# Kernel optimization log

Measured on AMD Instinct MI355X. Metric: run time of the kernel, lower is better.

The kernel has to match this reference:

```python
import jax, jax.numpy as jnp
from jax import lax
import numpy as np

B, L, C, H, W = 2, 5, 32, 48, 176
NUM_ITER = 1  # args['num_iteration']


def _affine_grid(M, Ho, Wo):
    # torch F.affine_grid, align_corners=False. M: (..., 2, 3) -> (..., Ho, Wo, 2)
    xs = (2.0 * jnp.arange(Wo, dtype=M.dtype) + 1.0) / Wo - 1.0
    ys = (2.0 * jnp.arange(Ho, dtype=M.dtype) + 1.0) / Ho - 1.0
    X, Y = jnp.meshgrid(xs, ys)  # (Ho, Wo)
    base = jnp.stack([X, Y, jnp.ones_like(X)], axis=-1)  # (Ho, Wo, 3)
    return jnp.einsum('...ij,hwj->...hwi', M, base)


def _grid_sample(img, grid):
    # torch F.grid_sample bilinear, zero padding, align_corners=False.
    # img: (C, H, W), grid: (Ho, Wo, 2) normalized coords -> (C, Ho, Wo)
    Ci, Hi, Wi = img.shape
    ix = ((grid[..., 0] + 1.0) * Wi - 1.0) * 0.5
    iy = ((grid[..., 1] + 1.0) * Hi - 1.0) * 0.5
    x0 = jnp.floor(ix)
    y0 = jnp.floor(iy)
    wx = ix - x0
    wy = iy - y0

    def tap(xf, yf):
        valid = ((xf >= 0) & (xf <= Wi - 1) & (yf >= 0) & (yf <= Hi - 1)).astype(img.dtype)
        xi = jnp.clip(xf, 0, Wi - 1).astype(jnp.int32)
        yi = jnp.clip(yf, 0, Hi - 1).astype(jnp.int32)
        return img[:, yi, xi] * valid  # (C, Ho, Wo)

    return (tap(x0, y0) * (1 - wx) * (1 - wy)
            + tap(x0 + 1, y0) * wx * (1 - wy)
            + tap(x0, y0 + 1) * (1 - wx) * wy
            + tap(x0 + 1, y0 + 1) * wx * wy)


_warp_batch = jax.vmap(_grid_sample)


def setup_inputs() -> dict:
    key = jax.random.key(0)
    ks = jax.random.split(key, 6)
    x = jax.random.normal(ks[0], (B * L, C, H, W), dtype=jnp.float32)
    record_len = jnp.full((B,), L, dtype=jnp.int64)
    eye = jnp.array([[1.0, 0.0, 0.0], [0.0, 1.0, 0.0]], dtype=jnp.float32)
    M = eye + 0.1 * jax.random.normal(ks[1], (B, L, L, 2, 3), dtype=jnp.float32)
    msg_w = jax.random.normal(ks[2], (C, 2 * C, 3, 3), dtype=jnp.float32) * (1.0 / np.sqrt(2 * C * 9))
    msg_b = jnp.zeros((C,), dtype=jnp.float32)
    mlp_w = jax.random.normal(ks[3], (C, C), dtype=jnp.float32) * (1.0 / np.sqrt(C))
    mlp_b = jnp.zeros((C,), dtype=jnp.float32)
    return {"x": x, "record_len": record_len, "normalized_affine_matrix": M,
            "msg_w": msg_w, "msg_b": msg_b, "mlp_w": mlp_w, "mlp_b": mlp_b}


def reference(x, record_len, normalized_affine_matrix, msg_w, msg_b, mlp_w, mlp_b):
    M = normalized_affine_matrix
    feat = x.reshape(B, L, C, H, W)  # regroup (record_len == L per batch)

    grids = _affine_grid(M, H, W).reshape(B * L * L, H, W, 2)

    # roi mask: warp an all-ones image with each pairwise transform
    ones_img = jnp.ones((1, H, W), dtype=x.dtype)
    mask = jax.vmap(lambda g: _grid_sample(ones_img, g))(grids)
    mask = mask.reshape(B, L, L, 1, H, W)

    for _ in range(NUM_ITER):
        # warped[b,i,j] = warp(feat[b,j], M[b,i,j])
        imgs = jnp.broadcast_to(feat[:, None], (B, L, L, C, H, W)).reshape(B * L * L, C, H, W)
        warped = _warp_batch(imgs, grids).reshape(B, L, L, C, H, W)
        ego = jnp.broadcast_to(feat[:, :, None], (B, L, L, C, H, W))
        cat = jnp.concatenate([warped, ego], axis=3).reshape(B * L * L, 2 * C, H, W)
        msg = lax.conv_general_dilated(cat, msg_w, (1, 1), ((1, 1), (1, 1)),
                                       dimension_numbers=('NCHW', 'OIHW', 'NCHW'))
        msg = msg + msg_b[None, :, None, None]
        msg = msg.reshape(B, L, L, C, H, W) * mask
        agg = jnp.max(msg, axis=2)  # 'max' agg over neighbors j -> (B, L, C, H, W)
        feat = feat + agg  # gru_flag=False branch

    out = feat[:, 0]  # ego agent feature, (B, C, H, W)
    out = jnp.einsum('bchw,dc->bdhw', out, mlp_w) + mlp_b[None, :, None, None]
    return out
```

## Files before the change

### kernel.cpp

```cpp
#include <hip/hip_runtime.h>
#include <hip/hip_bf16.h>
#include <math.h>

#define BB 2
#define LL 5
#define CC 32
#define HH 48
#define WW 176
#define HWs (HH * WW)
#define BL (BB * LL)

typedef __attribute__((ext_vector_type(8))) short bf16x8;
typedef __attribute__((ext_vector_type(4))) float f32x4;

__device__ __forceinline__ unsigned short f2bf(float v) {
    __hip_bfloat16 h = __float2bfloat16(v);
    return *reinterpret_cast<unsigned short*>(&h);
}
__device__ __forceinline__ float bf2f(unsigned short u) {
    __hip_bfloat16 h = *reinterpret_cast<__hip_bfloat16*>(&u);
    return __bfloat162float(h);
}

__device__ __forceinline__ void bilin_weights(const float* __restrict__ Mp, int h, int w,
                                              int& o00, int& o10, int& o01, int& o11,
                                              float& a00, float& a10, float& a01, float& a11)
{
    float xs = (2.0f * (float)w + 1.0f) / (float)WW - 1.0f;
    float ys = (2.0f * (float)h + 1.0f) / (float)HH - 1.0f;
    float gx = Mp[0] * xs + Mp[1] * ys + Mp[2];
    float gy = Mp[3] * xs + Mp[4] * ys + Mp[5];
    float ix = ((gx + 1.0f) * (float)WW - 1.0f) * 0.5f;
    float iy = ((gy + 1.0f) * (float)HH - 1.0f) * 0.5f;
    float x0f = floorf(ix), y0f = floorf(iy);
    float wx = ix - x0f, wy = iy - y0f;
    float x1f = x0f + 1.0f, y1f = y0f + 1.0f;
    bool vx0 = (x0f >= 0.0f) && (x0f <= (float)(WW - 1));
    bool vx1 = (x1f >= 0.0f) && (x1f <= (float)(WW - 1));
    bool vy0 = (y0f >= 0.0f) && (y0f <= (float)(HH - 1));
    bool vy1 = (y1f >= 0.0f) && (y1f <= (float)(HH - 1));
    int xi0 = (int)fminf(fmaxf(x0f, 0.0f), (float)(WW - 1));
    int xi1 = (int)fminf(fmaxf(x1f, 0.0f), (float)(WW - 1));
    int yi0 = (int)fminf(fmaxf(y0f, 0.0f), (float)(HH - 1));
    int yi1 = (int)fminf(fmaxf(y1f, 0.0f), (float)(HH - 1));
    o00 = yi0 * WW + xi0;
    o10 = yi0 * WW + xi1;
    o01 = yi1 * WW + xi0;
    o11 = yi1 * WW + xi1;
    a00 = (vx0 && vy0) ? (1.0f - wx) * (1.0f - wy) : 0.0f;
    a10 = (vx1 && vy0) ? wx * (1.0f - wy) : 0.0f;
    a01 = (vx0 && vy1) ? (1.0f - wx) * wy : 0.0f;
    a11 = (vx1 && vy1) ? wx * wy : 0.0f;
}

__global__ __launch_bounds__(256) void k_prep(const float* __restrict__ x,
                                              const float* __restrict__ M,
                                              const float* __restrict__ msg_w,
                                              const float* __restrict__ mlp_w,
                                              unsigned short* __restrict__ warpedcl,
                                              unsigned short* __restrict__ egocl,
                                              float* __restrict__ maskb,
                                              unsigned short* __restrict__ Wp,
                                              unsigned short* __restrict__ Wp2)
{
    int y = blockIdx.y;
    if (y < BL) {
        int pix = blockIdx.x * 256 + threadIdx.x;
        int cg  = blockIdx.z;
        int w = pix % WW, h = pix / WW;
        int b = y / LL, j = y % LL;
        const float* Mp = M + (size_t)(b * LL * LL + j) * 6;
        int o00, o10, o01, o11;
        float a00, a10, a01, a11;
        bilin_weights(Mp, h, w, o00, o10, o01, o11, a00, a10, a01, a11);
        if (cg == 0)
            maskb[(size_t)y * HWs + pix] = a00 + a10 + a01 + a11;
        const float* img = x + (size_t)y * CC * HWs + (size_t)cg * 8 * HWs;
        bf16x8 v8;
#pragma unroll
        for (int c = 0; c < 8; ++c) {
            const float* ip = img + (size_t)c * HWs;
            float v = a00 * ip[o00] + a10 * ip[o10] + a01 * ip[o01] + a11 * ip[o11];
            v8[c] = (short)f2bf(v);
        }
        *(bf16x8*)(warpedcl + ((size_t)y * HWs + pix) * CC + cg * 8) = v8;
    } else if (y < BL + BB) {
        int b = y - BL;
        int pix = blockIdx.x * 256 + threadIdx.x;
        int cg  = blockIdx.z;
        const float* img = x + (size_t)(b * LL) * CC * HWs + (size_t)cg * 8 * HWs;
        bf16x8 v8;
#pragma unroll
        for (int c = 0; c < 8; ++c)
            v8[c] = (short)f2bf(img[(size_t)c * HWs + pix]);
        *(bf16x8*)(egocl + ((size_t)b * HWs + pix) * CC + cg * 8) = v8;
    } else {
        int i = (blockIdx.z * gridDim.x + blockIdx.x) * 256 + threadIdx.x;
        if (i < 2 * 9 * 32 * 32) {
            int half = i / (9 * 32 * 32);
            int r    = i % (9 * 32 * 32);
            int tap  = r / (32 * 32);
            int r2   = r % (32 * 32);
            int oc   = r2 / 32;
            int ic   = r2 % 32;
            Wp[i] = f2bf(msg_w[(size_t)oc * 576 + (size_t)(half * 32 + ic) * 9 + tap]);
        } else if (i < 2 * 9 * 32 * 32 + 32 * 32) {
            int k = i - 2 * 9 * 32 * 32;
            Wp2[k] = f2bf(mlp_w[k]);
        }
    }
}

__global__ __launch_bounds__(256) void k_fused(const unsigned short* __restrict__ warpedcl,
                                               const unsigned short* __restrict__ egocl,
                                               const float* __restrict__ maskb,
                                               const unsigned short* __restrict__ Wp,
                                               const unsigned short* __restrict__ Wp2,
                                               const float* __restrict__ msg_b,
                                               const float* __restrict__ mlp_b,
                                               float* __restrict__ out)
{
    __shared__ float fl[64][33];
    int wv   = threadIdx.x >> 6;
    int lane = threadIdx.x & 63;
    int lo   = lane & 15;
    int kblk = lane >> 4;
    int b    = blockIdx.y;
    int p0   = blockIdx.x * 64 + wv * 16;
    int pf   = p0 + lo;
    int ph   = pf / WW, pw = pf % WW;

    int ps[9];
    unsigned vbits = 0;
#pragma unroll
    for (int tap = 0; tap < 9; ++tap) {
        int dy = tap / 3 - 1, dx = tap % 3 - 1;
        int hh = ph + dy, wwp = pw + dx;
        bool valid = (hh >= 0) && (hh < HH) && (wwp >= 0) && (wwp < WW);
        ps[tap] = valid ? (pf + dy * WW + dx) : pf;
        vbits |= (valid ? 1u : 0u) << tap;
    }
    const bf16x8 zero = {0, 0, 0, 0, 0, 0, 0, 0};

    bf16x8 Bw[9][2];
#pragma unroll
    for (int tap = 0; tap < 9; ++tap)
#pragma unroll
        for (int nt = 0; nt < 2; ++nt)
            Bw[tap][nt] = *(const bf16x8*)(Wp + ((size_t)(tap * 32 + nt * 16 + lo) * 32 + kblk * 8));

    f32x4 acce[2] = {};
    {
        const unsigned short* Ae = egocl + (size_t)b * HWs * CC;
#pragma unroll
        for (int tap = 0; tap < 9; ++tap) {
            bf16x8 Af = *(const bf16x8*)(Ae + (size_t)ps[tap] * CC + kblk * 8);
            if (!((vbits >> tap) & 1)) Af = zero;
#pragma unroll
            for (int nt = 0; nt < 2; ++nt) {
                bf16x8 Bf = *(const bf16x8*)(Wp + 9 * 32 * 32 + ((size_t)(tap * 32 + nt * 16 + lo) * 32 + kblk * 8));
                acce[nt] = __builtin_amdgcn_mfma_f32_16x16x32_bf16(Af, Bf, acce[nt], 0, 0, 0);
            }
        }
        float b0 = msg_b[lo], b1 = msg_b[16 + lo];
#pragma unroll
        for (int r = 0; r < 4; ++r) { acce[0][r] += b0; acce[1][r] += b1; }
    }

    f32x4 agg[2];
#pragma unroll
    for (int r = 0; r < 4; ++r) { agg[0][r] = -INFINITY; agg[1][r] = -INFINITY; }

    for (int j = 0; j < LL; ++j) {
        const unsigned short* Aw = warpedcl + (size_t)(b * LL + j) * HWs * CC;
        f32x4 acc[2] = {};
#pragma unroll
        for (int tap = 0; tap < 9; ++tap) {
            bf16x8 Af = *(const bf16x8*)(Aw + (size_t)ps[tap] * CC + kblk * 8);
            if (!((vbits >> tap) & 1)) Af = zero;
#pragma unroll
            for (int nt = 0; nt < 2; ++nt)
                acc[nt] = __builtin_amdgcn_mfma_f32_16x16x32_bf16(Af, Bw[tap][nt], acc[nt], 0, 0, 0);
        }
        float4 mk = *(const float4*)(maskb + (size_t)(b * LL + j) * HWs + p0 + kblk * 4);
        float mkr[4] = {mk.x, mk.y, mk.z, mk.w};
#pragma unroll
        for (int nt = 0; nt < 2; ++nt)
#pragma unroll
            for (int r = 0; r < 4; ++r)
                agg[nt][r] = fmaxf(agg[nt][r], (acc[nt][r] + acce[nt][r]) * mkr[r]);
    }

#pragma unroll
    for (int nt = 0; nt < 2; ++nt)
#pragma unroll
        for (int r = 0; r < 4; ++r) {
            int pixl = kblk * 4 + r;
            float skip = bf2f(egocl[((size_t)b * HWs + p0 + pixl) * CC + nt * 16 + lo]);
            float f = agg[nt][r] + skip;
            fl[wv * 16 + pixl][nt * 16 + lo] = f;
        }

    bf16x8 Afm;
#pragma unroll
    for (int e = 0; e < 8; ++e)
        Afm[e] = (short)f2bf(fl[wv * 16 + lo][kblk * 8 + e]);

#pragma unroll
    for (int nt2 = 0; nt2 < 2; ++nt2) {
        bf16x8 Bm = *(const bf16x8*)(Wp2 + ((size_t)(nt2 * 16 + lo) * 32 + kblk * 8));
        f32x4 om = {};
        om = __builtin_amdgcn_mfma_f32_16x16x32_bf16(Afm, Bm, om, 0, 0, 0);
        float mb2 = mlp_b[nt2 * 16 + lo];
        int d = nt2 * 16 + lo;
#pragma unroll
        for (int r = 0; r < 4; ++r)
            out[((size_t)b * CC + d) * HWs + p0 + kblk * 4 + r] = om[r] + mb2;
    }
}

extern "C" void kernel_launch(void* const* d_in, const int* in_sizes, int n_in,
                              void* d_out, int out_size, void* d_ws, size_t ws_size,
                              hipStream_t stream)
{
    (void)in_sizes; (void)n_in; (void)out_size; (void)ws_size;
    const float* x     = (const float*)d_in[0];
    const float* M     = (const float*)d_in[2];
    const float* msg_w = (const float*)d_in[3];
    const float* msg_b = (const float*)d_in[4];
    const float* mlp_w = (const float*)d_in[5];
    const float* mlp_b = (const float*)d_in[6];
    float* out = (float*)d_out;

    unsigned short* Wp       = (unsigned short*)d_ws;
    unsigned short* Wp2      = Wp + 2 * 9 * 32 * 32;
    unsigned short* warpedcl = Wp2 + 32 * 32;
    unsigned short* egocl    = warpedcl + (size_t)BL * HWs * CC;
    float*          maskb    = (float*)(egocl + (size_t)BB * HWs * CC);

    {
        dim3 g(HWs / 256, BL + BB + 1, 4);
        k_prep<<<g, 256, 0, stream>>>(x, M, msg_w, mlp_w,
                                      warpedcl, egocl, maskb, Wp, Wp2);
    }
    {
        dim3 g(HWs / 64, BB);
        k_fused<<<g, 256, 0, stream>>>(warpedcl, egocl, maskb, Wp, Wp2,
                                       msg_b, mlp_b, out);
    }
}
```

Measured before the change: 29.65 us.

## Stage conv weights in LDS, prefetch warped-feature taps, pair bilinear loads

```diff
diff --git a/kernel.cpp b/kernel.cpp
--- a/kernel.cpp
+++ b/kernel.cpp
@@ -9,6 +9,7 @@
 #define WW 176
 #define HWs (HH * WW)
 #define BL (BB * LL)
+#define WROW 36
 
 typedef __attribute__((ext_vector_type(8))) short bf16x8;
 typedef __attribute__((ext_vector_type(4))) float f32x4;
@@ -20,37 +21,6 @@
 __device__ __forceinline__ float bf2f(unsigned short u) {
     __hip_bfloat16 h = *reinterpret_cast<__hip_bfloat16*>(&u);
     return __bfloat162float(h);
-}
-
-__device__ __forceinline__ void bilin_weights(const float* __restrict__ Mp, int h, int w,
-                                              int& o00, int& o10, int& o01, int& o11,
-                                              float& a00, float& a10, float& a01, float& a11)
-{
-    float xs = (2.0f * (float)w + 1.0f) / (float)WW - 1.0f;
-    float ys = (2.0f * (float)h + 1.0f) / (float)HH - 1.0f;
-    float gx = Mp[0] * xs + Mp[1] * ys + Mp[2];
-    float gy = Mp[3] * xs + Mp[4] * ys + Mp[5];
-    float ix = ((gx + 1.0f) * (float)WW - 1.0f) * 0.5f;
-    float iy = ((gy + 1.0f) * (float)HH - 1.0f) * 0.5f;
-    float x0f = floorf(ix), y0f = floorf(iy);
-    float wx = ix - x0f, wy = iy - y0f;
-    float x1f = x0f + 1.0f, y1f = y0f + 1.0f;
-    bool vx0 = (x0f >= 0.0f) && (x0f <= (float)(WW - 1));
-    bool vx1 = (x1f >= 0.0f) && (x1f <= (float)(WW - 1));
-    bool vy0 = (y0f >= 0.0f) && (y0f <= (float)(HH - 1));
-    bool vy1 = (y1f >= 0.0f) && (y1f <= (float)(HH - 1));
-    int xi0 = (int)fminf(fmaxf(x0f, 0.0f), (float)(WW - 1));
-    int xi1 = (int)fminf(fmaxf(x1f, 0.0f), (float)(WW - 1));
-    int yi0 = (int)fminf(fmaxf(y0f, 0.0f), (float)(HH - 1));
-    int yi1 = (int)fminf(fmaxf(y1f, 0.0f), (float)(HH - 1));
-    o00 = yi0 * WW + xi0;
-    o10 = yi0 * WW + xi1;
-    o01 = yi1 * WW + xi0;
-    o11 = yi1 * WW + xi1;
-    a00 = (vx0 && vy0) ? (1.0f - wx) * (1.0f - wy) : 0.0f;
-    a10 = (vx1 && vy0) ? wx * (1.0f - wy) : 0.0f;
-    a01 = (vx0 && vy1) ? (1.0f - wx) * wy : 0.0f;
-    a11 = (vx1 && vy1) ? wx * wy : 0.0f;
 }
 
 __global__ __launch_bounds__(256) void k_prep(const float* __restrict__ x,
@@ -70,17 +40,50 @@
         int w = pix % WW, h = pix / WW;
         int b = y / LL, j = y % LL;
         const float* Mp = M + (size_t)(b * LL * LL + j) * 6;
-        int o00, o10, o01, o11;
-        float a00, a10, a01, a11;
-        bilin_weights(Mp, h, w, o00, o10, o01, o11, a00, a10, a01, a11);
+
+        float xs = (2.0f * (float)w + 1.0f) / (float)WW - 1.0f;
+        float ys = (2.0f * (float)h + 1.0f) / (float)HH - 1.0f;
+        float gx = Mp[0] * xs + Mp[1] * ys + Mp[2];
+        float gy = Mp[3] * xs + Mp[4] * ys + Mp[5];
+        float ix = ((gx + 1.0f) * (float)WW - 1.0f) * 0.5f;
+        float iy = ((gy + 1.0f) * (float)HH - 1.0f) * 0.5f;
+        float x0f = floorf(ix), y0f = floorf(iy);
+        float wx = ix - x0f, wy = iy - y0f;
+        float x1f = x0f + 1.0f, y1f = y0f + 1.0f;
+        bool vx0 = (x0f >= 0.0f) && (x0f <= (float)(WW - 1));
+        bool vx1 = (x1f >= 0.0f) && (x1f <= (float)(WW - 1));
+        bool vy0 = (y0f >= 0.0f) && (y0f <= (float)(HH - 1));
+        bool vy1 = (y1f >= 0.0f) && (y1f <= (float)(HH - 1));
+        int xi0 = (int)fminf(fmaxf(x0f, 0.0f), (float)(WW - 1));
+        int yi0 = (int)fminf(fmaxf(y0f, 0.0f), (float)(HH - 1));
+        int yi1 = (int)fminf(fmaxf(y1f, 0.0f), (float)(HH - 1));
+        float a00 = (vx0 && vy0) ? (1.0f - wx) * (1.0f - wy) : 0.0f;
+        float a10 = (vx1 && vy0) ? wx * (1.0f - wy) : 0.0f;
+        float a01 = (vx0 && vy1) ? (1.0f - wx) * wy : 0.0f;
+        float a11 = (vx1 && vy1) ? wx * wy : 0.0f;
+
         if (cg == 0)
             maskb[(size_t)y * HWs + pix] = a00 + a10 + a01 + a11;
+
+        bool adjx = (x0f >= 0.0f) && (x0f <= (float)(WW - 2));
+        int oL0 = yi0 * WW + xi0;
+        int oL1 = yi1 * WW + xi0;
+
         const float* img = x + (size_t)y * CC * HWs + (size_t)cg * 8 * HWs;
         bf16x8 v8;
 #pragma unroll
         for (int c = 0; c < 8; ++c) {
-            const float* ip = img + (size_t)c * HWs;
-            float v = a00 * ip[o00] + a10 * ip[o10] + a01 * ip[o01] + a11 * ip[o11];
+            const float* q = img + (size_t)c * HWs;
+            float v00, v10, v01, v11;
+            if (adjx) {
+                float2 u0 = *(const float2*)(q + oL0);
+                float2 u1 = *(const float2*)(q + oL1);
+                v00 = u0.x; v10 = u0.y; v01 = u1.x; v11 = u1.y;
+            } else {
+                v00 = v10 = q[oL0];
+                v01 = v11 = q[oL1];
+            }
+            float v = a00 * v00 + a10 * v10 + a01 * v01 + a11 * v11;
             v8[c] = (short)f2bf(v);
         }
         *(bf16x8*)(warpedcl + ((size_t)y * HWs + pix) * CC + cg * 8) = v8;
@@ -111,6 +114,18 @@
     }
 }
 
+__device__ __forceinline__ bf16x8 ldfrag(const unsigned short* __restrict__ wl,
+                                         int row, int kblk)
+{
+    const unsigned short* p = wl + row * WROW + kblk * 8;
+    ushort4 u0 = *(const ushort4*)(p);
+    ushort4 u1 = *(const ushort4*)(p + 4);
+    bf16x8 r;
+    r[0] = (short)u0.x; r[1] = (short)u0.y; r[2] = (short)u0.z; r[3] = (short)u0.w;
+    r[4] = (short)u1.x; r[5] = (short)u1.y; r[6] = (short)u1.z; r[7] = (short)u1.w;
+    return r;
+}
+
 __global__ __launch_bounds__(256) void k_fused(const unsigned short* __restrict__ warpedcl,
                                                const unsigned short* __restrict__ egocl,
                                                const float* __restrict__ maskb,
@@ -120,15 +135,26 @@
                                                const float* __restrict__ mlp_b,
                                                float* __restrict__ out)
 {
+    __shared__ unsigned short wlds[608 * WROW];
     __shared__ float fl[64][33];
-    int wv   = threadIdx.x >> 6;
-    int lane = threadIdx.x & 63;
-    int lo   = lane & 15;
-    int kblk = lane >> 4;
-    int b    = blockIdx.y;
-    int p0   = blockIdx.x * 64 + wv * 16;
-    int pf   = p0 + lo;
-    int ph   = pf / WW, pw = pf % WW;
+
+    const int tid  = threadIdx.x;
+    const int wv   = tid >> 6;
+    const int lane = tid & 63;
+    const int lo   = lane & 15;
+    const int kblk = lane >> 4;
+    const int b    = blockIdx.y;
+    const int p0   = blockIdx.x * 64 + wv * 16;
+    const int pf   = p0 + lo;
+    const int ph   = pf / WW, pw = pf % WW;
+
+#pragma unroll
+    for (int k = 0; k < 19; ++k) {
+        int g = k * 256 + tid;
+        ushort4 u = *(const ushort4*)(Wp + 4 * g);
+        int row = g >> 3, col = (g & 7) * 4;
+        *(ushort4*)(wlds + row * WROW + col) = u;
+    }
 
     int ps[9];
     unsigned vbits = 0;
@@ -142,48 +168,71 @@
     }
     const bf16x8 zero = {0, 0, 0, 0, 0, 0, 0, 0};
 
+    bf16x8 afe[9];
+    const unsigned short* Ae = egocl + (size_t)b * HWs * CC;
+#pragma unroll
+    for (int tap = 0; tap < 9; ++tap)
+        afe[tap] = *(const bf16x8*)(Ae + (size_t)ps[tap] * CC + kblk * 8);
+    float4 mks[LL];
+#pragma unroll
+    for (int j = 0; j < LL; ++j)
+        mks[j] = *(const float4*)(maskb + (size_t)(b * LL + j) * HWs + p0 + kblk * 4);
+
+    __syncthreads();
+
     bf16x8 Bw[9][2];
 #pragma unroll
     for (int tap = 0; tap < 9; ++tap)
 #pragma unroll
         for (int nt = 0; nt < 2; ++nt)
-            Bw[tap][nt] = *(const bf16x8*)(Wp + ((size_t)(tap * 32 + nt * 16 + lo) * 32 + kblk * 8));
+            Bw[tap][nt] = ldfrag(wlds, tap * 32 + nt * 16 + lo, kblk);
 
     f32x4 acce[2] = {};
+#pragma unroll
+    for (int tap = 0; tap < 9; ++tap) {
+        bf16x8 a = ((vbits >> tap) & 1) ? afe[tap] : zero;
+#pragma unroll
+        for (int nt = 0; nt < 2; ++nt) {
+            bf16x8 Be = ldfrag(wlds, 288 + tap * 32 + nt * 16 + lo, kblk);
+            acce[nt] = __builtin_amdgcn_mfma_f32_16x16x32_bf16(a, Be, acce[nt], 0, 0, 0);
+        }
+    }
     {
-        const unsigned short* Ae = egocl + (size_t)b * HWs * CC;
+        float b0 = msg_b[lo], b1 = msg_b[16 + lo];
+#pragma unroll
+        for (int r = 0; r < 4; ++r) { acce[0][r] += b0; acce[1][r] += b1; }
+    }
+
+    bf16x8 afw[3][9];
+#pragma unroll
+    for (int jj = 0; jj < 2; ++jj) {
+        const unsigned short* Aw = warpedcl + (size_t)(b * LL + jj) * HWs * CC;
+#pragma unroll
+        for (int tap = 0; tap < 9; ++tap)
+            afw[jj][tap] = *(const bf16x8*)(Aw + (size_t)ps[tap] * CC + kblk * 8);
+    }
+
+    f32x4 agg[2];
+#pragma unroll
+    for (int r = 0; r < 4; ++r) { agg[0][r] = -INFINITY; agg[1][r] = -INFINITY; }
+
+#pragma unroll
+    for (int j = 0; j < LL; ++j) {
+        if (j + 2 < LL) {
+            const unsigned short* Aw = warpedcl + (size_t)(b * LL + j + 2) * HWs * CC;
+#pragma unroll
+            for (int tap = 0; tap < 9; ++tap)
+                afw[(j + 2) % 3][tap] = *(const bf16x8*)(Aw + (size_t)ps[tap] * CC + kblk * 8);
+        }
+        f32x4 acc[2] = {};
 #pragma unroll
         for (int tap = 0; tap < 9; ++tap) {
-            bf16x8 Af = *(const bf16x8*)(Ae + (size_t)ps[tap] * CC + kblk * 8);
-            if (!((vbits >> tap) & 1)) Af = zero;
-#pragma unroll
-            for (int nt = 0; nt < 2; ++nt) {
-                bf16x8 Bf = *(const bf16x8*)(Wp + 9 * 32 * 32 + ((size_t)(tap * 32 + nt * 16 + lo) * 32 + kblk * 8));
-                acce[nt] = __builtin_amdgcn_mfma_f32_16x16x32_bf16(Af, Bf, acce[nt], 0, 0, 0);
-            }
-        }
-        float b0 = msg_b[lo], b1 = msg_b[16 + lo];
-#pragma unroll
-        for (int r = 0; r < 4; ++r) { acce[0][r] += b0; acce[1][r] += b1; }
-    }
-
-    f32x4 agg[2];
-#pragma unroll
-    for (int r = 0; r < 4; ++r) { agg[0][r] = -INFINITY; agg[1][r] = -INFINITY; }
-
-    for (int j = 0; j < LL; ++j) {
-        const unsigned short* Aw = warpedcl + (size_t)(b * LL + j) * HWs * CC;
-        f32x4 acc[2] = {};
-#pragma unroll
-        for (int tap = 0; tap < 9; ++tap) {
-            bf16x8 Af = *(const bf16x8*)(Aw + (size_t)ps[tap] * CC + kblk * 8);
-            if (!((vbits >> tap) & 1)) Af = zero;
+            bf16x8 a = ((vbits >> tap) & 1) ? afw[j % 3][tap] : zero;
 #pragma unroll
             for (int nt = 0; nt < 2; ++nt)
-                acc[nt] = __builtin_amdgcn_mfma_f32_16x16x32_bf16(Af, Bw[tap][nt], acc[nt], 0, 0, 0);
-        }
-        float4 mk = *(const float4*)(maskb + (size_t)(b * LL + j) * HWs + p0 + kblk * 4);
-        float mkr[4] = {mk.x, mk.y, mk.z, mk.w};
+                acc[nt] = __builtin_amdgcn_mfma_f32_16x16x32_bf16(a, Bw[tap][nt], acc[nt], 0, 0, 0);
+        }
+        float mkr[4] = {mks[j].x, mks[j].y, mks[j].z, mks[j].w};
 #pragma unroll
         for (int nt = 0; nt < 2; ++nt)
 #pragma unroll
@@ -197,10 +246,8 @@
         for (int r = 0; r < 4; ++r) {
             int pixl = kblk * 4 + r;
             float skip = bf2f(egocl[((size_t)b * HWs + p0 + pixl) * CC + nt * 16 + lo]);
-            float f = agg[nt][r] + skip;
-            fl[wv * 16 + pixl][nt * 16 + lo] = f;
-        }
-
+            fl[wv * 16 + pixl][nt * 16 + lo] = agg[nt][r] + skip;
+        }
     bf16x8 Afm;
 #pragma unroll
     for (int e = 0; e < 8; ++e)
@@ -208,7 +255,7 @@
 
 #pragma unroll
     for (int nt2 = 0; nt2 < 2; ++nt2) {
-        bf16x8 Bm = *(const bf16x8*)(Wp2 + ((size_t)(nt2 * 16 + lo) * 32 + kblk * 8));
+        bf16x8 Bm = ldfrag(wlds, 576 + nt2 * 16 + lo, kblk);
         f32x4 om = {};
         om = __builtin_amdgcn_mfma_f32_16x16x32_bf16(Afm, Bm, om, 0, 0, 0);
         float mb2 = mlp_b[nt2 * 16 + lo];
```

After: 27.37 us. -7.7%, faster.
